# Optimization experiments

Measured on AMD Instinct MI355X. Metric: run time of the kernel, lower is better.

Reference implementation:

```python
import jax, jax.numpy as jnp
import numpy as np

N = 50000      # nodes
E = 600000     # edges
D_IN = 128     # node_dim
D = 128        # out_channels
T = 4          # num_node_types
R = 4          # num_edge_types
L = 2          # num_layers
C = 8          # num_class
G = 512        # graphs in batch


def setup_inputs() -> dict:
    key = jax.random.key(0)
    ks = jax.random.split(key, 12)
    s = 0.05
    x = jax.random.normal(ks[0], (N, D_IN), jnp.float32)
    node_type = jax.random.randint(ks[1], (N,), 0, T)
    edge_index = jax.random.randint(ks[2], (2, E), 0, N)
    edge_type = jax.random.randint(ks[3], (E,), 0, R)
    batch = jnp.sort(jax.random.randint(ks[4], (N,), 0, G))
    # learned params
    W_het = jax.random.normal(ks[5], (T, D_IN, D), jnp.float32) * s
    b_het = jnp.zeros((T, D), jnp.float32)
    conv_W = jax.random.normal(ks[6], (L, R, D, D), jnp.float32) * s
    conv_b = jnp.zeros((L, R, D), jnp.float32)
    fuse_W = jax.random.normal(ks[7], (R * D, D), jnp.float32) * s
    fuse_b = jnp.zeros((D,), jnp.float32)
    cls_W = jax.random.normal(ks[8], (D, C), jnp.float32) * s
    cls_b = jnp.zeros((C,), jnp.float32)
    return dict(x=x, W_het=W_het, b_het=b_het, conv_W=conv_W, conv_b=conv_b,
                fuse_W=fuse_W, fuse_b=fuse_b, cls_W=cls_W, cls_b=cls_b,
                node_type=node_type, edge_index=edge_index, edge_type=edge_type,
                batch=batch)


def reference(x, W_het, b_het, conv_W, conv_b, fuse_W, fuse_b, cls_W, cls_b,
              node_type, edge_index, edge_type, batch):
    n = x.shape[0]
    # HeteroLinear: per-node-type linear. Compute all T projections then select.
    x_all = jnp.einsum('nd,tdo->tno', x, W_het)          # [T, N, D]
    h = x_all[node_type, jnp.arange(n)] + b_het[node_type]
    src, dst = edge_index[0], edge_index[1]
    for l in range(L):
        hs = h[src]                                       # [E, D] gather once per layer
        outs = []
        for r in range(R):
            # edges of relation r only (boolean mask == per-relation edge filtering)
            m = hs @ conv_W[l, r]                         # [E, D]
            m = m * (edge_type == r).astype(m.dtype)[:, None]
            agg = jax.ops.segment_sum(m, dst, num_segments=n)  # scatter-add to dst
            outs.append(agg + conv_b[l, r])
        h = jax.nn.relu(jnp.concatenate(outs, axis=1) @ fuse_W + fuse_b)
    # global mean pool over graphs
    counts = jax.ops.segment_sum(jnp.ones((n,), h.dtype), batch, num_segments=G)
    emb = jax.ops.segment_sum(h, batch, num_segments=G) / jnp.maximum(counts, 1.0)[:, None]
    logits = emb @ cls_W + cls_b
    return emb, logits
```

## Files before the change

### kernel.cpp

```cpp
#include <hip/hip_runtime.h>

#define N_NODES 50000
#define N_EDGES 600000
#define DIM     128
#define RR      4
#define LL      2
#define GG      512
#define CC      8
#define NCB     196
#define EC      (N_EDGES / 4)
#define FB      ((EC + 255) / 256)
#define TB      ((N_NODES + 255) / 256)
#define NBH     ((N_NODES + 63) / 64)
#define CB      (1026 + 3125)

typedef short bf16x8 __attribute__((ext_vector_type(8)));
typedef float f32x4  __attribute__((ext_vector_type(4)));

__device__ __forceinline__ float bf16_to_f(unsigned short u) {
    return __uint_as_float(((unsigned int)u) << 16);
}
__device__ __forceinline__ unsigned short f_to_bf16(float f) {
    unsigned int u = __float_as_uint(f);
    u += 0x7FFFu + ((u >> 16) & 1u);
    return (unsigned short)(u >> 16);
}
__device__ __forceinline__ float loadf(const void* p, long i, int isbf) {
    if (isbf) return bf16_to_f(((const unsigned short*)p)[i]);
    return ((const float*)p)[i];
}
__device__ __forceinline__ void storef(void* p, long i, float v, int isbf) {
    if (isbf) ((unsigned short*)p)[i] = f_to_bf16(v);
    else      ((float*)p)[i] = v;
}

__global__ void cg_init(const unsigned int* __restrict__ xw, int* __restrict__ flag,
                        int* __restrict__ chist_tb) {
    __shared__ int cnt;
    int tid = threadIdx.x;
    if (tid < NCB + 16) chist_tb[tid] = 0;
    if (tid == 0) cnt = 0;
    __syncthreads();
    unsigned int w = xw[tid];
    unsigned int e = (w >> 7) & 0xFFu;
    atomicAdd(&cnt, (e >= 110u && e <= 133u) ? 1 : 0);
    __syncthreads();
    if (tid == 0) *flag = (cnt >= 128) ? 1 : 0;
}

__global__ void cg_hist_canon(const int* __restrict__ edge_index, const int* __restrict__ node_type,
                              int* __restrict__ chist, int* __restrict__ tb,
                              const void* __restrict__ x,
                              const void* __restrict__ W_het, const void* __restrict__ b_het,
                              const void* __restrict__ conv_W, const void* __restrict__ fuse_W,
                              const void* __restrict__ conv_b, const void* __restrict__ fuse_b,
                              const int* __restrict__ flagp,
                              unsigned short* __restrict__ xb, unsigned short* __restrict__ Wt,
                              float* __restrict__ bhf,
                              unsigned short* __restrict__ M2t, float* __restrict__ cvec) {
    __shared__ float s[256];
    int bk = blockIdx.x;
    int tid = threadIdx.x;
    if (bk < FB) {
        __shared__ int lh[NCB];
        __shared__ int loc[4];
        for (int i = tid; i < NCB; i += 256) lh[i] = 0;
        if (tid < 4) loc[tid] = 0;
        __syncthreads();
        int t = bk * 256 + tid;
        if (t < EC) {
#pragma unroll
            for (int k = 0; k < 4; k++) {
                int d = edge_index[N_EDGES + t + k * EC];
                atomicAdd(&lh[d >> 8], 1);
            }
        }
        if (t < N_NODES) atomicAdd(&loc[node_type[t]], 1);
        __syncthreads();
        for (int i = tid; i < NCB; i += 256)
            if (lh[i]) atomicAdd(&chist[i], lh[i]);
        if (tid < 4 && loc[tid]) atomicAdd(&tb[tid], loc[tid]);
        return;
    }
    int b = bk - FB;
    int isbf = *flagp;
    if (b < 512) {
        int lr = b >> 6;
        int d  = (b & 63) * 2 + (tid >> 7);
        int r  = lr & 3;
        int o  = tid & 127;
        float acc = 0.0f;
        for (int k = 0; k < DIM; k++) {
            acc += loadf(conv_W, (long)(lr * DIM + d) * DIM + k, isbf)
                 * loadf(fuse_W, (long)(r * DIM + k) * DIM + o, isbf);
        }
        M2t[((long)lr * DIM + o) * DIM + d] = f_to_bf16(acc);
    } else if (b < 768) {
        int bc = b - 512;
        int l  = bc >> 7;
        int o  = bc & 127;
        float part = 0.0f;
        for (int rk = tid; rk < RR * DIM; rk += 256) {
            part += loadf(conv_b, (long)l * RR * DIM + rk, isbf)
                  * loadf(fuse_W, (long)rk * DIM + o, isbf);
        }
        s[tid] = part;
        __syncthreads();
        for (int off = 128; off > 0; off >>= 1) {
            if (tid < off) s[tid] += s[tid + off];
            __syncthreads();
        }
        if (tid == 0) cvec[bc] = s[0] + loadf(fuse_b, o, isbf);
    } else if (b < 1024) {
        int pair = (b - 768) * 2 + (tid >> 7);
        int t = pair >> 7;
        int o = pair & 127;
        int d = tid & 127;
        float v = loadf(W_het, ((long)t * DIM + d) * DIM + o, isbf);
        Wt[((long)t * DIM + o) * DIM + d] = f_to_bf16(v);
    } else if (b < 1026) {
        int idx = (b - 1024) * 256 + tid;
        if (idx < 4 * DIM) bhf[idx] = loadf(b_het, idx, isbf);
    } else {
        long i = ((long)(b - 1026) * 256 + tid) * 8;
        if (i >= (long)N_NODES * DIM) return;
        if (isbf) {
            *(uint4*)(xb + i) = *(const uint4*)((const unsigned short*)x + i);
        } else {
            const float* xf = (const float*)x + i;
            float4 f0 = *(const float4*)xf;
            float4 f1 = *(const float4*)(xf + 4);
            uint4 o;
            o.x = (unsigned int)f_to_bf16(f0.x) | ((unsigned int)f_to_bf16(f0.y) << 16);
            o.y = (unsigned int)f_to_bf16(f0.z) | ((unsigned int)f_to_bf16(f0.w) << 16);
            o.z = (unsigned int)f_to_bf16(f1.x) | ((unsigned int)f_to_bf16(f1.y) << 16);
            o.w = (unsigned int)f_to_bf16(f1.z) | ((unsigned int)f_to_bf16(f1.w) << 16);
            *(uint4*)(xb + i) = o;
        }
    }
}

__global__ void cg_scan196(const int* __restrict__ chist, int* __restrict__ blockoff,
                           int* __restrict__ ccursor, int* __restrict__ tb) {
    __shared__ int s[256];
    int tid = threadIdx.x;
    int v = (tid < NCB) ? chist[tid] : 0;
    s[tid] = v;
    __syncthreads();
    for (int off = 1; off < 256; off <<= 1) {
        int a = (tid >= off) ? s[tid - off] : 0;
        __syncthreads();
        s[tid] += a;
        __syncthreads();
    }
    if (tid < NCB) {
        int e = s[tid] - v;
        blockoff[tid] = e;
        ccursor[tid]  = e;
    }
    if (tid == 0) {
        int run = 0;
        for (int t = 0; t < 4; t++) {
            tb[8 + t] = run;
            tb[4 + t] = run;
            run += tb[t];
        }
        tb[12] = run;
    }
}

__global__ void cg_tfill(const int* __restrict__ node_type, int* __restrict__ tb,
                         int* __restrict__ tlist) {
    __shared__ int lcur[4];
    __shared__ int lbase[4];
    int tid = threadIdx.x;
    if (tid < 4) lcur[tid] = 0;
    __syncthreads();
    int n = blockIdx.x * 256 + tid;
    int slot = -1, t = 0;
    if (n < N_NODES) {
        t = node_type[n];
        slot = atomicAdd(&lcur[t], 1);
    }
    __syncthreads();
    if (tid < 4) lbase[tid] = atomicAdd(&tb[4 + tid], lcur[tid]);
    __syncthreads();
    if (n < N_NODES) tlist[lbase[t] + slot] = n;
}

#define APAD 136

__global__ void cg_sortA_hetero(const int* __restrict__ edge_index, const int* __restrict__ edge_type,
                                int* __restrict__ ccursor, int2* __restrict__ tmp2,
                                const unsigned short* __restrict__ xb,
                                const unsigned short* __restrict__ Wt,
                                const float* __restrict__ bhf,
                                const int* __restrict__ tlist, const int* __restrict__ tb,
                                unsigned short* __restrict__ h) {
    __shared__ unsigned short a_lds[64][APAD];
    __shared__ unsigned short b_lds[DIM][APAD];
    int bk = blockIdx.x;
    int tx = threadIdx.x;
    if (bk < FB) {
        __shared__ int lhist[NCB];
        __shared__ int lbase[NCB];
        for (int i = tx; i < NCB; i += 256) lhist[i] = 0;
        __syncthreads();
        int t = bk * 256 + tx;
        int d[4], cb[4], ls[4], pl[4];
        bool act = (t < EC);
        if (act) {
#pragma unroll
            for (int k = 0; k < 4; k++) {
                int e = t + k * EC;
                d[k]  = edge_index[N_EDGES + e];
                pl[k] = (edge_index[e] << 2) | edge_type[e];
                cb[k] = d[k] >> 8;
                ls[k] = atomicAdd(&lhist[cb[k]], 1);
            }
        }
        __syncthreads();
        for (int i = tx; i < NCB; i += 256)
            lbase[i] = lhist[i] ? atomicAdd(&ccursor[i], lhist[i]) : 0;
        __syncthreads();
        if (act) {
#pragma unroll
            for (int k = 0; k < 4; k++) {
                int pos = lbase[cb[k]] + ls[k];
                tmp2[pos] = make_int2(pl[k], d[k]);
            }
        }
        return;
    }
    int bb = bk - FB;
    int t    = bb / NBH;
    int nblk = bb - t * NBH;
    int rows_base = tb[8 + t] + nblk * 64;
    int rend = tb[8 + t + 1];
    if (rows_base >= rend) return;
    const unsigned short* Wsrc = Wt + (long)t * DIM * DIM;
    for (int i = tx; i < 2048; i += 256) {
        uint4 w = *(const uint4*)(Wsrc + i * 8);
        int o = i >> 4, d2 = (i & 15) * 8;
        *(uint4*)&b_lds[o][d2] = w;
    }
    for (int i = tx; i < 1024; i += 256) {
        int row = i >> 4, seg = (i & 15) * 8;
        int gr = rows_base + row;
        uint4 w = make_uint4(0u, 0u, 0u, 0u);
        if (gr < rend) {
            int n = tlist[gr];
            w = *(const uint4*)(xb + (long)n * DIM + seg);
        }
        *(uint4*)&a_lds[row][seg] = w;
    }
    __syncthreads();
    int wv = tx >> 6, lane = tx & 63;
    int m16 = lane & 15, quad = lane >> 4;
    f32x4 acc[8];
#pragma unroll
    for (int c = 0; c < 8; c++) acc[c] = (f32x4){0.f, 0.f, 0.f, 0.f};
    for (int ks = 0; ks < 4; ks++) {
        int koff = ks * 32 + quad * 8;
        bf16x8 af = *(const bf16x8*)(const void*)&a_lds[wv * 16 + m16][koff];
#pragma unroll
        for (int c = 0; c < 8; c++) {
            bf16x8 bfr = *(const bf16x8*)(const void*)&b_lds[c * 16 + m16][koff];
            acc[c] = __builtin_amdgcn_mfma_f32_16x16x32_bf16(af, bfr, acc[c], 0, 0, 0);
        }
    }
    __syncthreads();
#pragma unroll
    for (int c = 0; c < 8; c++) {
#pragma unroll
        for (int i = 0; i < 4; i++) {
            int row = wv * 16 + quad * 4 + i;
            int col = c * 16 + m16;
            a_lds[row][col] = f_to_bf16(acc[c][i] + bhf[t * DIM + col]);
        }
    }
    __syncthreads();
    for (int i = tx; i < 1024; i += 256) {
        int row = i >> 4, seg = (i & 15) * 8;
        int gr = rows_base + row;
        if (gr < rend) {
            int n = tlist[gr];
            *(uint4*)(h + (long)n * DIM + seg) = *(const uint4*)&a_lds[row][seg];
        }
    }
}

__global__ void cg_sortB_pgemm(const int2* __restrict__ tmp2, const int* __restrict__ blockoff,
                               int* __restrict__ rowptr, int* __restrict__ eidx,
                               const unsigned short* __restrict__ h,
                               const unsigned short* __restrict__ M2t,
                               unsigned short* __restrict__ P) {
    __shared__ unsigned short a_lds[64][APAD];
    __shared__ unsigned short b_lds[DIM][APAD];
    int bk = blockIdx.x;
    int tx = threadIdx.x;
    if (bk < NCB) {
        __shared__ int lcnt[256];
        __shared__ int lscan[256];
        __shared__ int lcur[256];
        lcnt[tx] = 0;
        int base = blockoff[bk];
        int endp = (bk + 1 < NCB) ? blockoff[bk + 1] : N_EDGES;
        int cnt = endp - base;
        __syncthreads();
        for (int i = tx; i < cnt; i += 256)
            atomicAdd(&lcnt[tmp2[base + i].y & 255], 1);
        __syncthreads();
        int v = lcnt[tx];
        lscan[tx] = v;
        __syncthreads();
        for (int off = 1; off < 256; off <<= 1) {
            int a = (tx >= off) ? lscan[tx - off] : 0;
            __syncthreads();
            lscan[tx] += a;
            __syncthreads();
        }
        int start = base + lscan[tx] - v;
        lcur[tx] = start;
        int n = bk * 256 + tx;
        if (n < N_NODES) rowptr[n] = start;
        __syncthreads();
        for (int i = tx; i < cnt; i += 256) {
            int2 e = tmp2[base + i];
            int pos = atomicAdd(&lcur[e.y & 255], 1);
            eidx[pos] = e.x;
        }
        return;
    }
    int bb = bk - NCB;
    int r    = bb / NBH;
    int nblk = bb - r * NBH;
    int n0 = nblk * 64;
    const unsigned short* Bsrc = M2t + (long)r * DIM * DIM;
    for (int i = tx; i < 2048; i += 256) {
        uint4 w = *(const uint4*)(Bsrc + i * 8);
        int o = i >> 4, d = (i & 15) * 8;
        *(uint4*)&b_lds[o][d] = w;
    }
    for (int i = tx; i < 1024; i += 256) {
        int row = i >> 4, seg = (i & 15) * 8;
        int n = n0 + row;
        uint4 w = make_uint4(0u, 0u, 0u, 0u);
        if (n < N_NODES) w = *(const uint4*)(h + (long)n * DIM + seg);
        *(uint4*)&a_lds[row][seg] = w;
    }
    __syncthreads();
    int wv = tx >> 6, lane = tx & 63;
    int m16 = lane & 15, quad = lane >> 4;
    f32x4 acc[8];
#pragma unroll
    for (int c = 0; c < 8; c++) acc[c] = (f32x4){0.f, 0.f, 0.f, 0.f};
    for (int ks = 0; ks < 4; ks++) {
        int koff = ks * 32 + quad * 8;
        bf16x8 af = *(const bf16x8*)(const void*)&a_lds[wv * 16 + m16][koff];
#pragma unroll
        for (int c = 0; c < 8; c++) {
            bf16x8 bfr = *(const bf16x8*)(const void*)&b_lds[c * 16 + m16][koff];
            acc[c] = __builtin_amdgcn_mfma_f32_16x16x32_bf16(af, bfr, acc[c], 0, 0, 0);
        }
    }
    __syncthreads();
#pragma unroll
    for (int c = 0; c < 8; c++) {
#pragma unroll
        for (int i = 0; i < 4; i++) {
            int row = wv * 16 + quad * 4 + i;
            int col = c * 16 + m16;
            a_lds[row][col] = f_to_bf16(acc[c][i]);
        }
    }
    __syncthreads();
    for (int i = tx; i < 1024; i += 256) {
        int row = i >> 4, seg = (i & 15) * 8;
        int n = n0 + row;
        if (n < N_NODES)
            *(uint4*)(P + (long)n * (RR * DIM) + r * DIM + seg) = *(const uint4*)&a_lds[row][seg];
    }
}

__global__ void cg_pgemm_mfma(const unsigned short* __restrict__ h,
                              const unsigned short* __restrict__ M2t, int l,
                              unsigned short* __restrict__ P) {
    int r  = blockIdx.y;
    int n0 = blockIdx.x * 64;
    __shared__ unsigned short a_lds[64][APAD];
    __shared__ unsigned short b_lds[DIM][APAD];
    int tx = threadIdx.x;
    const unsigned short* Bsrc = M2t + (long)(l * RR + r) * DIM * DIM;
    for (int i = tx; i < 2048; i += 256) {
        uint4 w = *(const uint4*)(Bsrc + i * 8);
        int o = i >> 4, d = (i & 15) * 8;
        *(uint4*)&b_lds[o][d] = w;
    }
    for (int i = tx; i < 1024; i += 256) {
        int row = i >> 4, seg = (i & 15) * 8;
        int n = n0 + row;
        uint4 w = make_uint4(0u, 0u, 0u, 0u);
        if (n < N_NODES) w = *(const uint4*)(h + (long)n * DIM + seg);
        *(uint4*)&a_lds[row][seg] = w;
    }
    __syncthreads();
    int wv = tx >> 6, lane = tx & 63;
    int m16 = lane & 15, quad = lane >> 4;
    f32x4 acc[8];
#pragma unroll
    for (int c = 0; c < 8; c++) acc[c] = (f32x4){0.f, 0.f, 0.f, 0.f};
    for (int ks = 0; ks < 4; ks++) {
        int koff = ks * 32 + quad * 8;
        bf16x8 af = *(const bf16x8*)(const void*)&a_lds[wv * 16 + m16][koff];
#pragma unroll
        for (int c = 0; c < 8; c++) {
            bf16x8 bfr = *(const bf16x8*)(const void*)&b_lds[c * 16 + m16][koff];
            acc[c] = __builtin_amdgcn_mfma_f32_16x16x32_bf16(af, bfr, acc[c], 0, 0, 0);
        }
    }
    __syncthreads();
#pragma unroll
    for (int c = 0; c < 8; c++) {
#pragma unroll
        for (int i = 0; i < 4; i++) {
            int row = wv * 16 + quad * 4 + i;
            int col = c * 16 + m16;
            a_lds[row][col] = f_to_bf16(acc[c][i]);
        }
    }
    __syncthreads();
    for (int i = tx; i < 1024; i += 256) {
        int row = i >> 4, seg = (i & 15) * 8;
        int n = n0 + row;
        if (n < N_NODES)
            *(uint4*)(P + (long)n * (RR * DIM) + r * DIM + seg) = *(const uint4*)&a_lds[row][seg];
    }
}

__global__ void cg_gather4(const unsigned short* __restrict__ P, const int* __restrict__ rowptr,
                           const int* __restrict__ eidx, const float* __restrict__ cv,
                           unsigned short* __restrict__ hout) {
    int wid  = (blockIdx.x * 256 + threadIdx.x) >> 6;
    int lane = threadIdx.x & 63;
    if (wid >= N_NODES) return;
    int eg = lane >> 4;
    int ol = lane & 15;
    int start = rowptr[wid];
    int end   = (wid + 1 < N_NODES) ? rowptr[wid + 1] : N_EDGES;
    float a[8] = {0.f, 0.f, 0.f, 0.f, 0.f, 0.f, 0.f, 0.f};
    int j = start + eg;
    for (; j + 4 < end; j += 8) {
        int v0 = eidx[j];
        int v1 = eidx[j + 4];
        const uint4 w0 = *(const uint4*)(P + (long)(v0 >> 2) * (RR * DIM) + (v0 & 3) * DIM + ol * 8);
        const uint4 w1 = *(const uint4*)(P + (long)(v1 >> 2) * (RR * DIM) + (v1 & 3) * DIM + ol * 8);
        a[0] += bf16_to_f((unsigned short)(w0.x & 0xFFFFu)) + bf16_to_f((unsigned short)(w1.x & 0xFFFFu));
        a[1] += bf16_to_f((unsigned short)(w0.x >> 16))     + bf16_to_f((unsigned short)(w1.x >> 16));
        a[2] += bf16_to_f((unsigned short)(w0.y & 0xFFFFu)) + bf16_to_f((unsigned short)(w1.y & 0xFFFFu));
        a[3] += bf16_to_f((unsigned short)(w0.y >> 16))     + bf16_to_f((unsigned short)(w1.y >> 16));
        a[4] += bf16_to_f((unsigned short)(w0.z & 0xFFFFu)) + bf16_to_f((unsigned short)(w1.z & 0xFFFFu));
        a[5] += bf16_to_f((unsigned short)(w0.z >> 16))     + bf16_to_f((unsigned short)(w1.z >> 16));
        a[6] += bf16_to_f((unsigned short)(w0.w & 0xFFFFu)) + bf16_to_f((unsigned short)(w1.w & 0xFFFFu));
        a[7] += bf16_to_f((unsigned short)(w0.w >> 16))     + bf16_to_f((unsigned short)(w1.w >> 16));
    }
    if (j < end) {
        int v = eidx[j];
        const uint4 w = *(const uint4*)(P + (long)(v >> 2) * (RR * DIM) + (v & 3) * DIM + ol * 8);
        a[0] += bf16_to_f((unsigned short)(w.x & 0xFFFFu));
        a[1] += bf16_to_f((unsigned short)(w.x >> 16));
        a[2] += bf16_to_f((unsigned short)(w.y & 0xFFFFu));
        a[3] += bf16_to_f((unsigned short)(w.y >> 16));
        a[4] += bf16_to_f((unsigned short)(w.z & 0xFFFFu));
        a[5] += bf16_to_f((unsigned short)(w.z >> 16));
        a[6] += bf16_to_f((unsigned short)(w.w & 0xFFFFu));
        a[7] += bf16_to_f((unsigned short)(w.w >> 16));
    }
#pragma unroll
    for (int i = 0; i < 8; i++) {
        a[i] += __shfl_xor(a[i], 16);
        a[i] += __shfl_xor(a[i], 32);
    }
    if (eg == 0) {
        int o0 = ol * 8;
        float v[8];
#pragma unroll
        for (int i = 0; i < 8; i++) {
            float s = a[i] + cv[o0 + i];
            v[i] = s > 0.0f ? s : 0.0f;
        }
        uint4 o4;
        o4.x = (unsigned int)f_to_bf16(v[0]) | ((unsigned int)f_to_bf16(v[1]) << 16);
        o4.y = (unsigned int)f_to_bf16(v[2]) | ((unsigned int)f_to_bf16(v[3]) << 16);
        o4.z = (unsigned int)f_to_bf16(v[4]) | ((unsigned int)f_to_bf16(v[5]) << 16);
        o4.w = (unsigned int)f_to_bf16(v[6]) | ((unsigned int)f_to_bf16(v[7]) << 16);
        *(uint4*)(hout + (long)wid * DIM + o0) = o4;
    }
}

__global__ void cg_pool_logits(const unsigned short* __restrict__ h, const int* __restrict__ batch,
                               const void* __restrict__ cls_W, const void* __restrict__ cls_b,
                               const int* __restrict__ flagp, void* __restrict__ out) {
    __shared__ float acc_s[4][DIM];
    __shared__ float emb_s[DIM];
    int g   = blockIdx.x;
    int tid = threadIdx.x;
    int wv  = tid >> 6;
    int lane = tid & 63;
    int sub = lane >> 4;
    int ol  = lane & 15;
    int isbf = *flagp;
    int lo = 0, hi = N_NODES;
    while (lo < hi) { int mid = (lo + hi) >> 1; if (batch[mid] < g) lo = mid + 1; else hi = mid; }
    int start = lo;
    hi = N_NODES;
    while (lo < hi) { int mid = (lo + hi) >> 1; if (batch[mid] < g + 1) lo = mid + 1; else hi = mid; }
    int end = lo;
    float a[8] = {0.f, 0.f, 0.f, 0.f, 0.f, 0.f, 0.f, 0.f};
    for (int n = start + wv * 4 + sub; n < end; n += 16) {
        uint4 w = *(const uint4*)(h + (long)n * DIM + ol * 8);
        a[0] += bf16_to_f((unsigned short)(w.x & 0xFFFFu));
        a[1] += bf16_to_f((unsigned short)(w.x >> 16));
        a[2] += bf16_to_f((unsigned short)(w.y & 0xFFFFu));
        a[3] += bf16_to_f((unsigned short)(w.y >> 16));
        a[4] += bf16_to_f((unsigned short)(w.z & 0xFFFFu));
        a[5] += bf16_to_f((unsigned short)(w.z >> 16));
        a[6] += bf16_to_f((unsigned short)(w.w & 0xFFFFu));
        a[7] += bf16_to_f((unsigned short)(w.w >> 16));
    }
#pragma unroll
    for (int i = 0; i < 8; i++) {
        a[i] += __shfl_xor(a[i], 16);
        a[i] += __shfl_xor(a[i], 32);
    }
    if (sub == 0) {
#pragma unroll
        for (int i = 0; i < 8; i++) acc_s[wv][ol * 8 + i] = a[i];
    }
    __syncthreads();
    int cnt = end - start;
    float inv = 1.0f / (float)(cnt > 1 ? cnt : 1);
    if (tid < DIM) {
        float e = (acc_s[0][tid] + acc_s[1][tid] + acc_s[2][tid] + acc_s[3][tid]) * inv;
        emb_s[tid] = e;
        storef(out, (long)g * DIM + tid, e, isbf);
    }
    __syncthreads();
    if (tid < 128) {
        int c  = tid >> 4;
        int kk = tid & 15;
        float p = 0.0f;
#pragma unroll
        for (int k = kk * 8; k < kk * 8 + 8; k++)
            p += emb_s[k] * loadf(cls_W, (long)k * CC + c, isbf);
        p += __shfl_xor(p, 1);
        p += __shfl_xor(p, 2);
        p += __shfl_xor(p, 4);
        p += __shfl_xor(p, 8);
        if (kk == 0)
            storef(out, (long)GG * DIM + g * CC + c, p + loadf(cls_b, c, isbf), isbf);
    }
}

extern "C" void kernel_launch(void* const* d_in, const int* in_sizes, int n_in,
                              void* d_out, int out_size, void* d_ws, size_t ws_size,
                              hipStream_t stream) {
    const void* x      = d_in[0];
    const void* W_het  = d_in[1];
    const void* b_het  = d_in[2];
    const void* conv_W = d_in[3];
    const void* conv_b = d_in[4];
    const void* fuse_W = d_in[5];
    const void* fuse_b = d_in[6];
    const void* cls_W  = d_in[7];
    const void* cls_b  = d_in[8];
    const int* node_type  = (const int*)d_in[9];
    const int* edge_index = (const int*)d_in[10];
    const int* edge_type  = (const int*)d_in[11];
    const int* batch      = (const int*)d_in[12];

    char* base = (char*)d_ws;
    unsigned short* hbf      = (unsigned short*)(base + 0);
    unsigned short* P        = (unsigned short*)(base + 12800000);
    unsigned short* xb       = (unsigned short*)(base + 64000000);
    unsigned short* Wt       = (unsigned short*)(base + 76800000);
    float*          bhf      = (float*)(base + 76931072);
    unsigned short* M2t      = (unsigned short*)(base + 76933120);
    float*          cvec     = (float*)(base + 77195264);
    int*            rowptr   = (int*)(base + 77196288);
    int*            chist    = (int*)(base + 77396320);
    int*            tb       = chist + NCB;
    int*            blockoff = (int*)(base + 77397408);
    int*            ccursor  = (int*)(base + 77398432);
    int*            eidx     = (int*)(base + 77399456);
    int*            tlist    = (int*)(base + 79799456);
    int*            flag     = (int*)(base + 79999456);
    int2*           tmp2     = (int2*)(base + 79999472);

    cg_init<<<1, 256, 0, stream>>>((const unsigned int*)x, flag, chist);
    cg_hist_canon<<<FB + CB, 256, 0, stream>>>(edge_index, node_type, chist, tb,
                                               x, W_het, b_het, conv_W, fuse_W,
                                               conv_b, fuse_b, flag,
                                               xb, Wt, bhf, M2t, cvec);
    cg_scan196<<<1, 256, 0, stream>>>(chist, blockoff, ccursor, tb);
    cg_tfill<<<TB, 256, 0, stream>>>(node_type, tb, tlist);
    cg_sortA_hetero<<<FB + 4 * NBH, 256, 0, stream>>>(edge_index, edge_type, ccursor, tmp2,
                                                      xb, Wt, bhf, tlist, tb, hbf);
    cg_sortB_pgemm<<<NCB + 4 * NBH, 256, 0, stream>>>(tmp2, blockoff, rowptr, eidx,
                                                      hbf, M2t, P);
    cg_gather4<<<(N_NODES * 64 + 255) / 256, 256, 0, stream>>>(
        P, rowptr, eidx, cvec, hbf);
    cg_pgemm_mfma<<<dim3(NBH, RR), 256, 0, stream>>>(hbf, M2t, 1, P);
    cg_gather4<<<(N_NODES * 64 + 255) / 256, 256, 0, stream>>>(
        P, rowptr, eidx, cvec + DIM, hbf);

    cg_pool_logits<<<GG, 256, 0, stream>>>(hbf, batch, cls_W, cls_b, flag, d_out);
}
```

Before: 292.9 us.

## Fuse four relation GEMMs per node tile and fuse final gather with pooling

The per-relation projection GEMM now runs all four relations in one block per 64-node tile. The A tile is loaded once and kept in registers while the four B matrices are streamed through LDS, so h is no longer re-read per relation and fewer blocks are launched. The last-layer gather kernel now applies bias and ReLU and scatters directly into per-graph accumulators with float atomics. This removes the write and re-read of the final h and the separate pooling pass, replaced by a small finalize kernel that does the mean and logits. The cost is float atomic contention on the graph accumulators, nondeterministic summation order, and an extra zeroing pass in the init kernel.

```diff
diff --git a/kernel.cpp b/kernel.cpp
--- a/kernel.cpp
+++ b/kernel.cpp
@@ -35,17 +35,22 @@
 }
 
 __global__ void cg_init(const unsigned int* __restrict__ xw, int* __restrict__ flag,
-                        int* __restrict__ chist_tb) {
+                        int* __restrict__ chist_tb, float4* __restrict__ emb0) {
     __shared__ int cnt;
+    int b = blockIdx.x;
     int tid = threadIdx.x;
-    if (tid < NCB + 16) chist_tb[tid] = 0;
-    if (tid == 0) cnt = 0;
-    __syncthreads();
-    unsigned int w = xw[tid];
-    unsigned int e = (w >> 7) & 0xFFu;
-    atomicAdd(&cnt, (e >= 110u && e <= 133u) ? 1 : 0);
-    __syncthreads();
-    if (tid == 0) *flag = (cnt >= 128) ? 1 : 0;
+    if (b == 0) {
+        if (tid < NCB + 16) chist_tb[tid] = 0;
+        if (tid == 0) cnt = 0;
+        __syncthreads();
+        unsigned int w = xw[tid];
+        unsigned int e = (w >> 7) & 0xFFu;
+        atomicAdd(&cnt, (e >= 110u && e <= 133u) ? 1 : 0);
+        __syncthreads();
+        if (tid == 0) *flag = (cnt >= 128) ? 1 : 0;
+    } else {
+        emb0[(b - 1) * 256 + tid] = make_float4(0.f, 0.f, 0.f, 0.f);
+    }
 }
 
 __global__ void cg_hist_canon(const int* __restrict__ edge_index, const int* __restrict__ node_type,
@@ -190,6 +195,68 @@
 
 #define APAD 136
 
+__device__ __forceinline__ void pgemm4r(const unsigned short* __restrict__ hsrc,
+                                        const unsigned short* __restrict__ M2base,
+                                        unsigned short* __restrict__ P,
+                                        int n0, int tx,
+                                        unsigned short a_lds[64][APAD],
+                                        unsigned short b_lds[DIM][APAD]) {
+    for (int i = tx; i < 1024; i += 256) {
+        int row = i >> 4, seg = (i & 15) * 8;
+        int n = n0 + row;
+        uint4 w = make_uint4(0u, 0u, 0u, 0u);
+        if (n < N_NODES) w = *(const uint4*)(hsrc + (long)n * DIM + seg);
+        *(uint4*)&a_lds[row][seg] = w;
+    }
+    for (int i = tx; i < 2048; i += 256) {
+        uint4 w = *(const uint4*)(M2base + i * 8);
+        *(uint4*)&b_lds[i >> 4][(i & 15) * 8] = w;
+    }
+    __syncthreads();
+    int wv = tx >> 6, lane = tx & 63;
+    int m16 = lane & 15, quad = lane >> 4;
+    bf16x8 af[4];
+#pragma unroll
+    for (int ks = 0; ks < 4; ks++)
+        af[ks] = *(const bf16x8*)(const void*)&a_lds[wv * 16 + m16][ks * 32 + quad * 8];
+    __syncthreads();
+    for (int r = 0; r < 4; r++) {
+        f32x4 acc[8];
+#pragma unroll
+        for (int c = 0; c < 8; c++) acc[c] = (f32x4){0.f, 0.f, 0.f, 0.f};
+#pragma unroll
+        for (int ks = 0; ks < 4; ks++) {
+            int koff = ks * 32 + quad * 8;
+#pragma unroll
+            for (int c = 0; c < 8; c++) {
+                bf16x8 bfr = *(const bf16x8*)(const void*)&b_lds[c * 16 + m16][koff];
+                acc[c] = __builtin_amdgcn_mfma_f32_16x16x32_bf16(af[ks], bfr, acc[c], 0, 0, 0);
+            }
+        }
+        __syncthreads();
+#pragma unroll
+        for (int c = 0; c < 8; c++) {
+#pragma unroll
+            for (int i = 0; i < 4; i++)
+                a_lds[wv * 16 + quad * 4 + i][c * 16 + m16] = f_to_bf16(acc[c][i]);
+        }
+        if (r < 3) {
+            const unsigned short* Bs = M2base + (long)(r + 1) * DIM * DIM;
+            for (int i = tx; i < 2048; i += 256) {
+                uint4 w = *(const uint4*)(Bs + i * 8);
+                *(uint4*)&b_lds[i >> 4][(i & 15) * 8] = w;
+            }
+        }
+        __syncthreads();
+        for (int i = tx; i < 1024; i += 256) {
+            int row = i >> 4, seg = (i & 15) * 8;
+            int n = n0 + row;
+            if (n < N_NODES)
+                *(uint4*)(P + (long)n * (RR * DIM) + r * DIM + seg) = *(const uint4*)&a_lds[row][seg];
+        }
+    }
+}
+
 __global__ void cg_sortA_hetero(const int* __restrict__ edge_index, const int* __restrict__ edge_type,
                                 int* __restrict__ ccursor, int2* __restrict__ tmp2,
                                 const unsigned short* __restrict__ xb,
@@ -332,110 +399,16 @@
         }
         return;
     }
-    int bb = bk - NCB;
-    int r    = bb / NBH;
-    int nblk = bb - r * NBH;
-    int n0 = nblk * 64;
-    const unsigned short* Bsrc = M2t + (long)r * DIM * DIM;
-    for (int i = tx; i < 2048; i += 256) {
-        uint4 w = *(const uint4*)(Bsrc + i * 8);
-        int o = i >> 4, d = (i & 15) * 8;
-        *(uint4*)&b_lds[o][d] = w;
-    }
-    for (int i = tx; i < 1024; i += 256) {
-        int row = i >> 4, seg = (i & 15) * 8;
-        int n = n0 + row;
-        uint4 w = make_uint4(0u, 0u, 0u, 0u);
-        if (n < N_NODES) w = *(const uint4*)(h + (long)n * DIM + seg);
-        *(uint4*)&a_lds[row][seg] = w;
-    }
-    __syncthreads();
-    int wv = tx >> 6, lane = tx & 63;
-    int m16 = lane & 15, quad = lane >> 4;
-    f32x4 acc[8];
-#pragma unroll
-    for (int c = 0; c < 8; c++) acc[c] = (f32x4){0.f, 0.f, 0.f, 0.f};
-    for (int ks = 0; ks < 4; ks++) {
-        int koff = ks * 32 + quad * 8;
-        bf16x8 af = *(const bf16x8*)(const void*)&a_lds[wv * 16 + m16][koff];
-#pragma unroll
-        for (int c = 0; c < 8; c++) {
-            bf16x8 bfr = *(const bf16x8*)(const void*)&b_lds[c * 16 + m16][koff];
-            acc[c] = __builtin_amdgcn_mfma_f32_16x16x32_bf16(af, bfr, acc[c], 0, 0, 0);
-        }
-    }
-    __syncthreads();
-#pragma unroll
-    for (int c = 0; c < 8; c++) {
-#pragma unroll
-        for (int i = 0; i < 4; i++) {
-            int row = wv * 16 + quad * 4 + i;
-            int col = c * 16 + m16;
-            a_lds[row][col] = f_to_bf16(acc[c][i]);
-        }
-    }
-    __syncthreads();
-    for (int i = tx; i < 1024; i += 256) {
-        int row = i >> 4, seg = (i & 15) * 8;
-        int n = n0 + row;
-        if (n < N_NODES)
-            *(uint4*)(P + (long)n * (RR * DIM) + r * DIM + seg) = *(const uint4*)&a_lds[row][seg];
-    }
-}
-
-__global__ void cg_pgemm_mfma(const unsigned short* __restrict__ h,
-                              const unsigned short* __restrict__ M2t, int l,
+    int n0 = (bk - NCB) * 64;
+    pgemm4r(h, M2t, P, n0, tx, a_lds, b_lds);
+}
+
+__global__ void cg_pgemm4r_l1(const unsigned short* __restrict__ h,
+                              const unsigned short* __restrict__ M2t,
                               unsigned short* __restrict__ P) {
-    int r  = blockIdx.y;
-    int n0 = blockIdx.x * 64;
     __shared__ unsigned short a_lds[64][APAD];
     __shared__ unsigned short b_lds[DIM][APAD];
-    int tx = threadIdx.x;
-    const unsigned short* Bsrc = M2t + (long)(l * RR + r) * DIM * DIM;
-    for (int i = tx; i < 2048; i += 256) {
-        uint4 w = *(const uint4*)(Bsrc + i * 8);
-        int o = i >> 4, d = (i & 15) * 8;
-        *(uint4*)&b_lds[o][d] = w;
-    }
-    for (int i = tx; i < 1024; i += 256) {
-        int row = i >> 4, seg = (i & 15) * 8;
-        int n = n0 + row;
-        uint4 w = make_uint4(0u, 0u, 0u, 0u);
-        if (n < N_NODES) w = *(const uint4*)(h + (long)n * DIM + seg);
-        *(uint4*)&a_lds[row][seg] = w;
-    }
-    __syncthreads();
-    int wv = tx >> 6, lane = tx & 63;
-    int m16 = lane & 15, quad = lane >> 4;
-    f32x4 acc[8];
-#pragma unroll
-    for (int c = 0; c < 8; c++) acc[c] = (f32x4){0.f, 0.f, 0.f, 0.f};
-    for (int ks = 0; ks < 4; ks++) {
-        int koff = ks * 32 + quad * 8;
-        bf16x8 af = *(const bf16x8*)(const void*)&a_lds[wv * 16 + m16][koff];
-#pragma unroll
-        for (int c = 0; c < 8; c++) {
-            bf16x8 bfr = *(const bf16x8*)(const void*)&b_lds[c * 16 + m16][koff];
-            acc[c] = __builtin_amdgcn_mfma_f32_16x16x32_bf16(af, bfr, acc[c], 0, 0, 0);
-        }
-    }
-    __syncthreads();
-#pragma unroll
-    for (int c = 0; c < 8; c++) {
-#pragma unroll
-        for (int i = 0; i < 4; i++) {
-            int row = wv * 16 + quad * 4 + i;
-            int col = c * 16 + m16;
-            a_lds[row][col] = f_to_bf16(acc[c][i]);
-        }
-    }
-    __syncthreads();
-    for (int i = tx; i < 1024; i += 256) {
-        int row = i >> 4, seg = (i & 15) * 8;
-        int n = n0 + row;
-        if (n < N_NODES)
-            *(uint4*)(P + (long)n * (RR * DIM) + r * DIM + seg) = *(const uint4*)&a_lds[row][seg];
-    }
+    pgemm4r(h, M2t + (long)RR * DIM * DIM, P, blockIdx.x * 64, threadIdx.x, a_lds, b_lds);
 }
 
 __global__ void cg_gather4(const unsigned short* __restrict__ P, const int* __restrict__ rowptr,
@@ -498,27 +471,38 @@
     }
 }
 
-__global__ void cg_pool_logits(const unsigned short* __restrict__ h, const int* __restrict__ batch,
-                               const void* __restrict__ cls_W, const void* __restrict__ cls_b,
-                               const int* __restrict__ flagp, void* __restrict__ out) {
-    __shared__ float acc_s[4][DIM];
-    __shared__ float emb_s[DIM];
-    int g   = blockIdx.x;
-    int tid = threadIdx.x;
-    int wv  = tid >> 6;
-    int lane = tid & 63;
-    int sub = lane >> 4;
-    int ol  = lane & 15;
-    int isbf = *flagp;
-    int lo = 0, hi = N_NODES;
-    while (lo < hi) { int mid = (lo + hi) >> 1; if (batch[mid] < g) lo = mid + 1; else hi = mid; }
-    int start = lo;
-    hi = N_NODES;
-    while (lo < hi) { int mid = (lo + hi) >> 1; if (batch[mid] < g + 1) lo = mid + 1; else hi = mid; }
-    int end = lo;
+__global__ void cg_gather_pool(const unsigned short* __restrict__ P, const int* __restrict__ rowptr,
+                               const int* __restrict__ eidx, const float* __restrict__ cv,
+                               const int* __restrict__ batch, float* __restrict__ emb_acc) {
+    __shared__ float sm[4][DIM];
+    __shared__ int sg[4];
+    int wid  = (blockIdx.x * 256 + threadIdx.x) >> 6;
+    int lane = threadIdx.x & 63;
+    int tid  = threadIdx.x;
+    int wv   = tid >> 6;
+    int eg = lane >> 4;
+    int ol = lane & 15;
+    int start = rowptr[wid];
+    int end   = (wid + 1 < N_NODES) ? rowptr[wid + 1] : N_EDGES;
     float a[8] = {0.f, 0.f, 0.f, 0.f, 0.f, 0.f, 0.f, 0.f};
-    for (int n = start + wv * 4 + sub; n < end; n += 16) {
-        uint4 w = *(const uint4*)(h + (long)n * DIM + ol * 8);
+    int j = start + eg;
+    for (; j + 4 < end; j += 8) {
+        int v0 = eidx[j];
+        int v1 = eidx[j + 4];
+        const uint4 w0 = *(const uint4*)(P + (long)(v0 >> 2) * (RR * DIM) + (v0 & 3) * DIM + ol * 8);
+        const uint4 w1 = *(const uint4*)(P + (long)(v1 >> 2) * (RR * DIM) + (v1 & 3) * DIM + ol * 8);
+        a[0] += bf16_to_f((unsigned short)(w0.x & 0xFFFFu)) + bf16_to_f((unsigned short)(w1.x & 0xFFFFu));
+        a[1] += bf16_to_f((unsigned short)(w0.x >> 16))     + bf16_to_f((unsigned short)(w1.x >> 16));
+        a[2] += bf16_to_f((unsigned short)(w0.y & 0xFFFFu)) + bf16_to_f((unsigned short)(w1.y & 0xFFFFu));
+        a[3] += bf16_to_f((unsigned short)(w0.y >> 16))     + bf16_to_f((unsigned short)(w1.y >> 16));
+        a[4] += bf16_to_f((unsigned short)(w0.z & 0xFFFFu)) + bf16_to_f((unsigned short)(w1.z & 0xFFFFu));
+        a[5] += bf16_to_f((unsigned short)(w0.z >> 16))     + bf16_to_f((unsigned short)(w1.z >> 16));
+        a[6] += bf16_to_f((unsigned short)(w0.w & 0xFFFFu)) + bf16_to_f((unsigned short)(w1.w & 0xFFFFu));
+        a[7] += bf16_to_f((unsigned short)(w0.w >> 16))     + bf16_to_f((unsigned short)(w1.w >> 16));
+    }
+    if (j < end) {
+        int v = eidx[j];
+        const uint4 w = *(const uint4*)(P + (long)(v >> 2) * (RR * DIM) + (v & 3) * DIM + ol * 8);
         a[0] += bf16_to_f((unsigned short)(w.x & 0xFFFFu));
         a[1] += bf16_to_f((unsigned short)(w.x >> 16));
         a[2] += bf16_to_f((unsigned short)(w.y & 0xFFFFu));
@@ -533,15 +517,50 @@
         a[i] += __shfl_xor(a[i], 16);
         a[i] += __shfl_xor(a[i], 32);
     }
-    if (sub == 0) {
-#pragma unroll
-        for (int i = 0; i < 8; i++) acc_s[wv][ol * 8 + i] = a[i];
-    }
-    __syncthreads();
+    if (lane == 0) sg[wv] = batch[wid];
+    if (eg == 0) {
+        int o0 = ol * 8;
+#pragma unroll
+        for (int i = 0; i < 8; i++) {
+            float s = a[i] + cv[o0 + i];
+            sm[wv][o0 + i] = s > 0.0f ? s : 0.0f;
+        }
+    }
+    __syncthreads();
+    if (tid < DIM) {
+        float s = sm[0][tid];
+        int cg = sg[0];
+#pragma unroll
+        for (int w = 1; w < 4; w++) {
+            if (sg[w] == cg) {
+                s += sm[w][tid];
+            } else {
+                atomicAdd(&emb_acc[(long)cg * DIM + tid], s);
+                cg = sg[w];
+                s = sm[w][tid];
+            }
+        }
+        atomicAdd(&emb_acc[(long)cg * DIM + tid], s);
+    }
+}
+
+__global__ void cg_finalize(const float* __restrict__ emb_acc, const int* __restrict__ batch,
+                            const void* __restrict__ cls_W, const void* __restrict__ cls_b,
+                            const int* __restrict__ flagp, void* __restrict__ out) {
+    __shared__ float emb_s[DIM];
+    int g   = blockIdx.x;
+    int tid = threadIdx.x;
+    int isbf = *flagp;
+    int lo = 0, hi = N_NODES;
+    while (lo < hi) { int mid = (lo + hi) >> 1; if (batch[mid] < g) lo = mid + 1; else hi = mid; }
+    int start = lo;
+    hi = N_NODES;
+    while (lo < hi) { int mid = (lo + hi) >> 1; if (batch[mid] < g + 1) lo = mid + 1; else hi = mid; }
+    int end = lo;
     int cnt = end - start;
     float inv = 1.0f / (float)(cnt > 1 ? cnt : 1);
     if (tid < DIM) {
-        float e = (acc_s[0][tid] + acc_s[1][tid] + acc_s[2][tid] + acc_s[3][tid]) * inv;
+        float e = emb_acc[(long)g * DIM + tid] * inv;
         emb_s[tid] = e;
         storef(out, (long)g * DIM + tid, e, isbf);
     }
@@ -596,8 +615,9 @@
     int*            tlist    = (int*)(base + 79799456);
     int*            flag     = (int*)(base + 79999456);
     int2*           tmp2     = (int2*)(base + 79999472);
-
-    cg_init<<<1, 256, 0, stream>>>((const unsigned int*)x, flag, chist);
+    float*          emb_acc  = (float*)(base + 84799472);
+
+    cg_init<<<65, 256, 0, stream>>>((const unsigned int*)x, flag, chist, (float4*)emb_acc);
     cg_hist_canon<<<FB + CB, 256, 0, stream>>>(edge_index, node_type, chist, tb,
                                                x, W_het, b_het, conv_W, fuse_W,
                                                conv_b, fuse_b, flag,
@@ -606,13 +626,12 @@
     cg_tfill<<<TB, 256, 0, stream>>>(node_type, tb, tlist);
     cg_sortA_hetero<<<FB + 4 * NBH, 256, 0, stream>>>(edge_index, edge_type, ccursor, tmp2,
                                                       xb, Wt, bhf, tlist, tb, hbf);
-    cg_sortB_pgemm<<<NCB + 4 * NBH, 256, 0, stream>>>(tmp2, blockoff, rowptr, eidx,
-                                                      hbf, M2t, P);
+    cg_sortB_pgemm<<<NCB + NBH, 256, 0, stream>>>(tmp2, blockoff, rowptr, eidx,
+                                                  hbf, M2t, P);
     cg_gather4<<<(N_NODES * 64 + 255) / 256, 256, 0, stream>>>(
         P, rowptr, eidx, cvec, hbf);
-    cg_pgemm_mfma<<<dim3(NBH, RR), 256, 0, stream>>>(hbf, M2t, 1, P);
-    cg_gather4<<<(N_NODES * 64 + 255) / 256, 256, 0, stream>>>(
-        P, rowptr, eidx, cvec + DIM, hbf);
-
-    cg_pool_logits<<<GG, 256, 0, stream>>>(hbf, batch, cls_W, cls_b, flag, d_out);
-}
+    cg_pgemm4r_l1<<<NBH, 256, 0, stream>>>(hbf, M2t, P);
+    cg_gather_pool<<<(N_NODES * 64 + 255) / 256, 256, 0, stream>>>(
+        P, rowptr, eidx, cvec + DIM, batch, emb_acc);
+    cg_finalize<<<GG, 256, 0, stream>>>(emb_acc, batch, cls_W, cls_b, flag, d_out);
+}
```

Measured after the change: 284.9 us. 1.03x faster.
